# Optimization experiments

Hardware: AMD Instinct MI355X
Metric: run time of the kernel (lower is better)

## Reference

```python
import jax, jax.numpy as jnp
import numpy as np

D_MODEL = 1024
N_HEADS = 16
D_K = D_MODEL // N_HEADS
MAX_SEQ = 2048
THETA = 10000.0


def _make_cos_sin():
    # cos_sin[i, k, 0] = cos(i / theta**(2k/d_k)), [.., 1] = sin(...)
    pos = np.arange(MAX_SEQ, dtype=np.float32)[:, None]
    k = np.arange(D_K // 2, dtype=np.float32)[None, :]
    ang = pos / (THETA ** (2.0 * k / D_K))
    return jnp.asarray(np.stack([np.cos(ang), np.sin(ang)], axis=-1), dtype=jnp.float32)


def setup_inputs() -> dict:
    key = jax.random.key(0)
    ks = jax.random.split(key, 5)
    std = 2.0 / (D_MODEL + D_MODEL)
    def w(k):
        return std * jax.random.truncated_normal(k, -3.0, 3.0, (D_MODEL, D_MODEL), dtype=jnp.float32)
    return {
        "x": jax.random.normal(ks[0], (4, 2048, D_MODEL), dtype=jnp.float32),
        "Wq": w(ks[1]),
        "Wk": w(ks[2]),
        "Wv": w(ks[3]),
        "Wo": w(ks[4]),
        "cos_sin": _make_cos_sin(),
        "token_positions": jnp.arange(2048, dtype=jnp.int32),
    }


def _rope(x, cos_sin, pos):
    # x: [B, H, S, d_k]; rotate consecutive pairs
    B, H, S, d = x.shape
    xt = x.reshape(B, H, S, d // 2, 2)
    cos = cos_sin[pos, :, 0]  # [S, d/2]
    sin = cos_sin[pos, :, 1]
    x0, x1 = xt[..., 0], xt[..., 1]
    r0 = cos * x0 - sin * x1
    r1 = sin * x0 + cos * x1
    return jnp.stack([r0, r1], axis=-1).reshape(B, H, S, d)


def reference(x, Wq, Wk, Wv, Wo, cos_sin, token_positions):
    B, S, D = x.shape
    H, d = N_HEADS, D_K
    def proj(W):
        y = jnp.einsum('bsi,oi->bso', x, W)
        return y.reshape(B, S, H, d).transpose(0, 2, 1, 3)  # [B,H,S,d]
    q = _rope(proj(Wq), cos_sin, token_positions)
    k = _rope(proj(Wk), cos_sin, token_positions)
    v = proj(Wv)
    scores = jnp.einsum('bhqd,bhkd->bhqk', q, k) / jnp.sqrt(jnp.float32(d))
    causal = jnp.tril(jnp.ones((S, S), dtype=bool))
    scores = jnp.where(causal, scores, -jnp.inf)
    attn = jax.nn.softmax(scores, axis=-1)
    out = jnp.einsum('bhqk,bhkd->bhqd', attn, v)
    out = out.transpose(0, 2, 1, 3).reshape(B, S, D)
    return jnp.einsum('bsi,oi->bso', out, Wo)
```

## Files before the change

### kernel.cpp

```cpp
#include <hip/hip_runtime.h>

constexpr int B_  = 4;
constexpr int S_  = 2048;
constexpr int D_  = 1024;
constexpr int H_  = 16;
constexpr int DK_ = 64;
constexpr int M_  = B_ * S_;

typedef __attribute__((ext_vector_type(8))) short short8;
typedef __attribute__((ext_vector_type(4))) float f32x4;
typedef __attribute__((ext_vector_type(4))) unsigned short us4;

__device__ __forceinline__ unsigned short f2b(float f) {
  unsigned int u = __float_as_uint(f);
  u += 0x7FFFu + ((u >> 16) & 1u);
  return (unsigned short)(u >> 16);
}
__device__ __forceinline__ float b2f(unsigned short h) {
  return __uint_as_float(((unsigned int)h) << 16);
}
__device__ __forceinline__ unsigned int cvtpk(float lo, float hi) {
  unsigned int w;
  asm("v_cvt_pk_bf16_f32 %0, %1, %2" : "=v"(w) : "v"(lo), "v"(hi));
  return w;
}
__device__ __forceinline__ float exp2v(float x) {
  float r;
  asm("v_exp_f32 %0, %1" : "=v"(r) : "v"(x));
  return r;
}

#define GLOAD16(g, l) __builtin_amdgcn_global_load_lds( \
    (const __attribute__((address_space(1))) unsigned int*)(g), \
    (__attribute__((address_space(3))) unsigned int*)(l), 16, 0, 0)

__global__ __launch_bounds__(256) void conv_kernel(
    const float* __restrict__ x,
    const float* __restrict__ wq, const float* __restrict__ wk, const float* __restrict__ wv,
    unsigned short* __restrict__ xb, unsigned short* __restrict__ wb)
{
  const int NX4 = (M_ * D_) / 4;
  const int NW4 = (3 * D_ * D_) / 4;
  int stride = gridDim.x * blockDim.x;
  for (int i = blockIdx.x * blockDim.x + threadIdx.x; i < NX4 + NW4; i += stride) {
    const float4* src; unsigned short* dst; int o;
    if (i < NX4) { src = (const float4*)x; dst = xb; o = i; }
    else {
      int wi = i - NX4;
      int mat = wi >> 18;
      o = wi & 262143;
      src = (const float4*)(mat == 0 ? wq : (mat == 1 ? wk : wv));
      dst = wb + mat * (D_ * D_);
    }
    float4 v = src[o];
    us4 r; r.x = f2b(v.x); r.y = f2b(v.y); r.z = f2b(v.z); r.w = f2b(v.w);
    *(us4*)(dst + o * 4) = r;
  }
}

__global__ __launch_bounds__(256) void conv_wo_kernel(
    const float* __restrict__ wo, unsigned short* __restrict__ wob)
{
  int i = blockIdx.x * 256 + threadIdx.x;
  float4 v = ((const float4*)wo)[i];
  us4 r; r.x = f2b(v.x); r.y = f2b(v.y); r.z = f2b(v.z); r.w = f2b(v.w);
  *(us4*)(wob + i * 4) = r;
}

__global__ __launch_bounds__(256) void gemm_qkv_kernel(
    const unsigned short* __restrict__ xb,
    const unsigned short* __restrict__ wb,
    const float* __restrict__ cs,
    const int* __restrict__ pos,
    unsigned short* __restrict__ qb,
    unsigned short* __restrict__ kb,
    unsigned short* __restrict__ vtb)
{
  __shared__ unsigned short As[128 * 32];
  __shared__ unsigned short Bs[128 * 32];
  const int tid  = threadIdx.x;
  const int lane = tid & 63;
  const int wid  = tid >> 6;
  const int wm = wid >> 1, wn = wid & 1;
  const int m0 = blockIdx.x * 128;
  const int n0 = blockIdx.y * 128;
  const int l15 = lane & 15, l4 = lane >> 4;

  const int c0 = tid;
  const int rA0 = c0 >> 2, cA0 = (c0 & 3) * 8;
  const int c1 = tid + 256;
  const int rA1 = c1 >> 2, cA1 = (c1 & 3) * 8;
  const int lb0 = (wid * 64) * 8;
  const int lb1 = (256 + wid * 64) * 8;

  f32x4 acc[4][4] = {};

  for (int t = 0; t < 32; ++t) {
    __syncthreads();
    GLOAD16(xb + (m0 + rA0) * D_ + t * 32 + cA0, &As[lb0]);
    GLOAD16(xb + (m0 + rA1) * D_ + t * 32 + cA1, &As[lb1]);
    GLOAD16(wb + (n0 + rA0) * D_ + t * 32 + cA0, &Bs[lb0]);
    GLOAD16(wb + (n0 + rA1) * D_ + t * 32 + cA1, &Bs[lb1]);
    __syncthreads();

    short8 af[4], bfr[4];
    #pragma unroll
    for (int mi = 0; mi < 4; ++mi) af[mi]  = *(const short8*)&As[(wm*64 + mi*16 + l15)*32 + l4*8];
    #pragma unroll
    for (int ni = 0; ni < 4; ++ni) bfr[ni] = *(const short8*)&Bs[(wn*64 + ni*16 + l15)*32 + l4*8];
    __builtin_amdgcn_s_setprio(1);
    #pragma unroll
    for (int mi = 0; mi < 4; ++mi)
      #pragma unroll
      for (int ni = 0; ni < 4; ++ni)
        acc[mi][ni] = __builtin_amdgcn_mfma_f32_16x16x32_bf16(af[mi], bfr[ni], acc[mi][ni], 0, 0, 0);
    __builtin_amdgcn_s_setprio(0);
  }

  const int bidx = m0 >> 11;
  const int sbase = (m0 & 2047) + wm * 64;

  if (n0 < 2048) {
    unsigned short* dst = (n0 < 1024) ? qb : kb;
    const int nn0 = n0 & 1023;
    const float2* cs2 = (const float2*)cs;
    const float sg = (l15 & 1) ? 1.0f : -1.0f;
    #pragma unroll
    for (int mi = 0; mi < 4; ++mi)
      #pragma unroll
      for (int j = 0; j < 4; ++j) {
        int s = sbase + mi*16 + l4*4 + j;
        int p = pos[s];
        #pragma unroll
        for (int ni = 0; ni < 4; ++ni) {
          int col = nn0 + wn*64 + ni*16 + l15;
          int h = col >> 6, dd = col & 63;
          float val = acc[mi][ni][j];
          float par = __shfl_xor(val, 1);
          float2 cv = cs2[p*32 + (dd >> 1)];
          float r = fmaf(cv.x, val, sg * cv.y * par);
          dst[((bidx*H_ + h)*S_ + s)*DK_ + dd] = f2b(r);
        }
      }
  } else {
    const int nn0 = n0 & 1023;
    const int hB = (nn0 + wn*64) >> 6;
    #pragma unroll
    for (int mi = 0; mi < 4; ++mi) {
      int s4 = sbase + mi*16 + l4*4;
      #pragma unroll
      for (int ni = 0; ni < 4; ++ni) {
        int dd = ni*16 + l15;
        uint2 w;
        w.x = cvtpk(acc[mi][ni][0], acc[mi][ni][1]);
        w.y = cvtpk(acc[mi][ni][2], acc[mi][ni][3]);
        *(uint2*)(vtb + ((bidx*H_ + hB)*DK_ + dd)*S_ + s4) = w;
      }
    }
  }
}

__global__ __launch_bounds__(256, 4) void attn_kernel(
    const unsigned short* __restrict__ qb,
    const unsigned short* __restrict__ kb,
    const unsigned short* __restrict__ vtb,
    unsigned short* __restrict__ ao)
{
  __shared__ unsigned short Ks[64][72];
  __shared__ unsigned short Vs[64][72];
  __shared__ unsigned short Ps[4][16][72];
  const int tid = threadIdx.x, lane = tid & 63, wid = tid >> 6;
  const int l15 = lane & 15, l4 = lane >> 4;

  const int id  = blockIdx.x;
  const int xcd = id & 7, jj2 = id >> 3;
  const int bh  = xcd * 8 + (jj2 & 7);
  const int qt  = 15 - (jj2 >> 3);
  const int q0  = qt * 128;
  const int nkt = 2 * qt + 2;

  const unsigned short* qp = qb  + bh * S_ * DK_;
  const unsigned short* kp = kb  + bh * S_ * DK_;
  const unsigned short* vp = vtb + bh * DK_ * S_;
  const int bidx = bh >> 4, h = bh & 15;

  const float QSC = 0.18033688f;
  short8 qf[2][2];
  #pragma unroll
  for (int y = 0; y < 2; ++y)
    #pragma unroll
    for (int kbk = 0; kbk < 2; ++kbk) {
      short8 raw = *(const short8*)(qp + (q0 + y*64 + wid*16 + l15)*DK_ + kbk*32 + l4*8);
      #pragma unroll
      for (int i = 0; i < 8; ++i) {
        float f = b2f((unsigned short)raw[i]) * QSC;
        raw[i] = (short)f2b(f);
      }
      qf[y][kbk] = raw;
    }

  f32x4 oacc[2][4] = {};
  float mrun[2] = {-1e30f, -1e30f}, lrun[2] = {0.0f, 0.0f};

  short8 kv[2], vv[2];
  #pragma unroll
  for (int jj = 0; jj < 2; ++jj) {
    int c = tid + jj * 256;
    int r = c >> 3, col = (c & 7) * 8;
    kv[jj] = *(const short8*)(kp + r*DK_ + col);
    vv[jj] = *(const short8*)(vp + r*S_ + col);
  }

  for (int kt = 0; kt < nkt; ++kt) {
    __syncthreads();
    #pragma unroll
    for (int jj = 0; jj < 2; ++jj) {
      int c = tid + jj * 256;
      int r = c >> 3, col = (c & 7) * 8;
      *(short8*)&Ks[r][col] = kv[jj];
      *(short8*)&Vs[r][col] = vv[jj];
    }
    __syncthreads();

    if (kt + 1 < nkt) {
      #pragma unroll
      for (int jj = 0; jj < 2; ++jj) {
        int c = tid + jj * 256;
        int r = c >> 3, col = (c & 7) * 8;
        kv[jj] = *(const short8*)(kp + ((kt+1)*64 + r)*DK_ + col);
        vv[jj] = *(const short8*)(vp + r*S_ + (kt+1)*64 + col);
      }
    }

    #pragma unroll
    for (int y = 0; y < 2; ++y) {
      if (kt > 2*qt + y) continue;

      f32x4 sc[4];
      __builtin_amdgcn_s_setprio(1);
      #pragma unroll
      for (int nb = 0; nb < 4; ++nb) {
        short8 k0 = *(const short8*)&Ks[nb*16 + l15][l4*8];
        short8 k1 = *(const short8*)&Ks[nb*16 + l15][32 + l4*8];
        f32x4 z = {};
        z = __builtin_amdgcn_mfma_f32_16x16x32_bf16(k0, qf[y][0], z, 0, 0, 0);
        z = __builtin_amdgcn_mfma_f32_16x16x32_bf16(k1, qf[y][1], z, 0, 0, 0);
        sc[nb] = z;
      }
      __builtin_amdgcn_s_setprio(0);

      if (kt == 2*qt + y) {
        const int qg = q0 + y*64 + wid*16 + l15;
        #pragma unroll
        for (int nb = 0; nb < 4; ++nb)
          #pragma unroll
          for (int j = 0; j < 4; ++j) {
            int kg = kt*64 + nb*16 + l4*4 + j;
            if (kg > qg) sc[nb][j] = -1e30f;
          }
      }

      float tm = sc[0][0];
      #pragma unroll
      for (int nb = 0; nb < 4; ++nb)
        #pragma unroll
        for (int j = 0; j < 4; ++j) tm = fmaxf(tm, sc[nb][j]);
      tm = fmaxf(tm, __shfl_xor(tm, 16));
      tm = fmaxf(tm, __shfl_xor(tm, 32));
      if (!__all(tm - mrun[y] <= 8.0f)) {
        float mnew = fmaxf(mrun[y], tm);
        float corr = exp2v(mrun[y] - mnew);
        mrun[y] = mnew;
        lrun[y] *= corr;
        #pragma unroll
        for (int j = 0; j < 4; ++j) {
          float cj = __shfl(corr, l4*4 + j);
          #pragma unroll
          for (int nb = 0; nb < 4; ++nb) oacc[y][nb][j] *= cj;
        }
      }
      float rs = 0.0f;
      #pragma unroll
      for (int nb = 0; nb < 4; ++nb)
        #pragma unroll
        for (int j = 0; j < 4; ++j) {
          float p = exp2v(sc[nb][j] - mrun[y]);
          sc[nb][j] = p;
          rs += p;
        }
      rs += __shfl_xor(rs, 16);
      rs += __shfl_xor(rs, 32);
      lrun[y] += rs;

      #pragma unroll
      for (int nb = 0; nb < 4; ++nb) {
        uint2 w;
        w.x = cvtpk(sc[nb][0], sc[nb][1]);
        w.y = cvtpk(sc[nb][2], sc[nb][3]);
        *(uint2*)&Ps[wid][l15][nb*16 + l4*4] = w;
      }
      asm volatile("s_waitcnt lgkmcnt(0)" ::: "memory");
      short8 pa0 = *(const short8*)&Ps[wid][l15][l4*8];
      short8 pa1 = *(const short8*)&Ps[wid][l15][32 + l4*8];

      __builtin_amdgcn_s_setprio(1);
      #pragma unroll
      for (int nb = 0; nb < 4; ++nb) {
        short8 v0 = *(const short8*)&Vs[nb*16 + l15][l4*8];
        short8 v1 = *(const short8*)&Vs[nb*16 + l15][32 + l4*8];
        oacc[y][nb] = __builtin_amdgcn_mfma_f32_16x16x32_bf16(pa0, v0, oacc[y][nb], 0, 0, 0);
        oacc[y][nb] = __builtin_amdgcn_mfma_f32_16x16x32_bf16(pa1, v1, oacc[y][nb], 0, 0, 0);
      }
      __builtin_amdgcn_s_setprio(0);
    }
  }

  #pragma unroll
  for (int y = 0; y < 2; ++y)
    #pragma unroll
    for (int j = 0; j < 4; ++j) {
      float lj = __shfl(lrun[y], l4*4 + j);
      float inv = 1.0f / lj;
      int row = q0 + y*64 + wid*16 + l4*4 + j;
      #pragma unroll
      for (int nb = 0; nb < 4; ++nb) {
        int dim = nb*16 + l15;
        ao[((bidx*S_ + row)*H_ + h)*DK_ + dim] = f2b(oacc[y][nb][j] * inv);
      }
    }
}

__global__ __launch_bounds__(256) void gemm_out_kernel(
    const unsigned short* __restrict__ ao,
    const unsigned short* __restrict__ wob,
    float* __restrict__ out)
{
  __shared__ unsigned short As[128 * 32];
  __shared__ unsigned short Bs[128 * 32];
  const int tid = threadIdx.x, lane = tid & 63, wid = tid >> 6;
  const int wm = wid >> 1, wn = wid & 1;
  const int m0 = blockIdx.x * 128, n0 = blockIdx.y * 128;
  const int l15 = lane & 15, l4 = lane >> 4;

  const int c0 = tid;
  const int rA0 = c0 >> 2, cA0 = (c0 & 3) * 8;
  const int c1 = tid + 256;
  const int rA1 = c1 >> 2, cA1 = (c1 & 3) * 8;
  const int lb0 = (wid * 64) * 8;
  const int lb1 = (256 + wid * 64) * 8;

  f32x4 acc[4][4] = {};

  for (int t = 0; t < 32; ++t) {
    __syncthreads();
    GLOAD16(ao  + (m0 + rA0) * D_ + t * 32 + cA0, &As[lb0]);
    GLOAD16(ao  + (m0 + rA1) * D_ + t * 32 + cA1, &As[lb1]);
    GLOAD16(wob + (n0 + rA0) * D_ + t * 32 + cA0, &Bs[lb0]);
    GLOAD16(wob + (n0 + rA1) * D_ + t * 32 + cA1, &Bs[lb1]);
    __syncthreads();

    short8 af[4], bfr[4];
    #pragma unroll
    for (int mi = 0; mi < 4; ++mi) af[mi]  = *(const short8*)&As[(wm*64 + mi*16 + l15)*32 + l4*8];
    #pragma unroll
    for (int ni = 0; ni < 4; ++ni) bfr[ni] = *(const short8*)&Bs[(wn*64 + ni*16 + l15)*32 + l4*8];
    __builtin_amdgcn_s_setprio(1);
    #pragma unroll
    for (int mi = 0; mi < 4; ++mi)
      #pragma unroll
      for (int ni = 0; ni < 4; ++ni)
        acc[mi][ni] = __builtin_amdgcn_mfma_f32_16x16x32_bf16(af[mi], bfr[ni], acc[mi][ni], 0, 0, 0);
    __builtin_amdgcn_s_setprio(0);
  }

  #pragma unroll
  for (int mi = 0; mi < 4; ++mi)
    #pragma unroll
    for (int ni = 0; ni < 4; ++ni)
      #pragma unroll
      for (int j = 0; j < 4; ++j) {
        int row = m0 + wm*64 + mi*16 + l4*4 + j;
        int col = n0 + wn*64 + ni*16 + l15;
        out[row * D_ + col] = acc[mi][ni][j];
      }
}

extern "C" void kernel_launch(void* const* d_in, const int* in_sizes, int n_in,
                              void* d_out, int out_size, void* d_ws, size_t ws_size,
                              hipStream_t stream)
{
  const float* x  = (const float*)d_in[0];
  const float* wq = (const float*)d_in[1];
  const float* wk = (const float*)d_in[2];
  const float* wv = (const float*)d_in[3];
  const float* wo = (const float*)d_in[4];
  const float* cs = (const float*)d_in[5];
  const int*  pos = (const int*)d_in[6];
  float* out = (float*)d_out;

  unsigned short* xb = (unsigned short*)d_out;
  unsigned short* wb = xb + M_ * D_;

  unsigned short* qb  = (unsigned short*)d_ws;
  unsigned short* kbf = qb  + M_ * D_;
  unsigned short* vtb = kbf + M_ * D_;
  unsigned short* aob = vtb + M_ * D_;
  unsigned short* wob = qb;

  conv_kernel<<<dim3(2048), dim3(256), 0, stream>>>(x, wq, wk, wv, xb, wb);
  gemm_qkv_kernel<<<dim3(64, 24), dim3(256), 0, stream>>>(xb, wb, cs, pos, qb, kbf, vtb);
  attn_kernel<<<dim3(1024), dim3(256), 0, stream>>>(qb, kbf, vtb, aob);
  conv_wo_kernel<<<dim3(1024), dim3(256), 0, stream>>>(wo, wob);
  gemm_out_kernel<<<dim3(64, 8), dim3(256), 0, stream>>>(aob, wob, out);

  (void)in_sizes; (void)n_in; (void)out_size; (void)ws_size;
}
```

Baseline: 201.9 us.

## Double-buffer GEMM LDS tiles with BK=64 and XOR swizzle

Both projection GEMMs (QKV and output) now stage 64-wide K tiles in double-buffered LDS. The next tile's global-to-LDS loads are issued before the current tile's MFMAs, so there is one barrier per iteration instead of two. Tile columns are XOR-swizzled by row to avoid LDS bank conflicts on the 128-byte row stride, and launch bounds request two blocks per CU. The cost is four times the LDS per block (64 KB), which may limit occupancy. It also relies on async loads not landing early in the buffer still being read.

```diff
diff --git a/kernel.cpp b/kernel.cpp
--- a/kernel.cpp
+++ b/kernel.cpp
@@ -67,7 +67,7 @@
   *(us4*)(wob + i * 4) = r;
 }
 
-__global__ __launch_bounds__(256) void gemm_qkv_kernel(
+__global__ __launch_bounds__(256, 2) void gemm_qkv_kernel(
     const unsigned short* __restrict__ xb,
     const unsigned short* __restrict__ wb,
     const float* __restrict__ cs,
@@ -76,8 +76,8 @@
     unsigned short* __restrict__ kb,
     unsigned short* __restrict__ vtb)
 {
-  __shared__ unsigned short As[128 * 32];
-  __shared__ unsigned short Bs[128 * 32];
+  __shared__ unsigned short As[2][128 * 64];
+  __shared__ unsigned short Bs[2][128 * 64];
   const int tid  = threadIdx.x;
   const int lane = tid & 63;
   const int wid  = tid >> 6;
@@ -85,36 +85,56 @@
   const int m0 = blockIdx.x * 128;
   const int n0 = blockIdx.y * 128;
   const int l15 = lane & 15, l4 = lane >> 4;
-
-  const int c0 = tid;
-  const int rA0 = c0 >> 2, cA0 = (c0 & 3) * 8;
-  const int c1 = tid + 256;
-  const int rA1 = c1 >> 2, cA1 = (c1 & 3) * 8;
-  const int lb0 = (wid * 64) * 8;
-  const int lb1 = (256 + wid * 64) * 8;
+  const int swz7 = l15 & 7;
+
+  int srow[4], sgcc[4], slds[4];
+  #pragma unroll
+  for (int j = 0; j < 4; ++j) {
+    int c = tid + j * 256;
+    srow[j] = c >> 3;
+    int cc  = c & 7;
+    sgcc[j] = cc ^ (srow[j] & 7);
+    slds[j] = (wid * 64 + j * 256) * 8;
+  }
 
   f32x4 acc[4][4] = {};
 
-  for (int t = 0; t < 32; ++t) {
+  #pragma unroll
+  for (int j = 0; j < 4; ++j) {
+    GLOAD16(xb + (m0 + srow[j]) * D_ + sgcc[j] * 8, &As[0][slds[j]]);
+    GLOAD16(wb + (n0 + srow[j]) * D_ + sgcc[j] * 8, &Bs[0][slds[j]]);
+  }
+  __syncthreads();
+
+  for (int t = 0; t < 16; ++t) {
+    const int cur = t & 1, nxt = cur ^ 1;
+    if (t < 15) {
+      const int kcol = (t + 1) * 64;
+      #pragma unroll
+      for (int j = 0; j < 4; ++j) {
+        GLOAD16(xb + (m0 + srow[j]) * D_ + kcol + sgcc[j] * 8, &As[nxt][slds[j]]);
+        GLOAD16(wb + (n0 + srow[j]) * D_ + kcol + sgcc[j] * 8, &Bs[nxt][slds[j]]);
+      }
+    }
+    const unsigned short* Ab = &As[cur][0];
+    const unsigned short* Bb = &Bs[cur][0];
+    #pragma unroll
+    for (int ks = 0; ks < 2; ++ks) {
+      const int cc = (ks * 4 + l4) ^ swz7;
+      short8 af[4], bfr[4];
+      #pragma unroll
+      for (int mi = 0; mi < 4; ++mi) af[mi]  = *(const short8*)&Ab[(wm*64 + mi*16 + l15)*64 + cc*8];
+      #pragma unroll
+      for (int ni = 0; ni < 4; ++ni) bfr[ni] = *(const short8*)&Bb[(wn*64 + ni*16 + l15)*64 + cc*8];
+      __builtin_amdgcn_s_setprio(1);
+      #pragma unroll
+      for (int mi = 0; mi < 4; ++mi)
+        #pragma unroll
+        for (int ni = 0; ni < 4; ++ni)
+          acc[mi][ni] = __builtin_amdgcn_mfma_f32_16x16x32_bf16(af[mi], bfr[ni], acc[mi][ni], 0, 0, 0);
+      __builtin_amdgcn_s_setprio(0);
+    }
     __syncthreads();
-    GLOAD16(xb + (m0 + rA0) * D_ + t * 32 + cA0, &As[lb0]);
-    GLOAD16(xb + (m0 + rA1) * D_ + t * 32 + cA1, &As[lb1]);
-    GLOAD16(wb + (n0 + rA0) * D_ + t * 32 + cA0, &Bs[lb0]);
-    GLOAD16(wb + (n0 + rA1) * D_ + t * 32 + cA1, &Bs[lb1]);
-    __syncthreads();
-
-    short8 af[4], bfr[4];
-    #pragma unroll
-    for (int mi = 0; mi < 4; ++mi) af[mi]  = *(const short8*)&As[(wm*64 + mi*16 + l15)*32 + l4*8];
-    #pragma unroll
-    for (int ni = 0; ni < 4; ++ni) bfr[ni] = *(const short8*)&Bs[(wn*64 + ni*16 + l15)*32 + l4*8];
-    __builtin_amdgcn_s_setprio(1);
-    #pragma unroll
-    for (int mi = 0; mi < 4; ++mi)
-      #pragma unroll
-      for (int ni = 0; ni < 4; ++ni)
-        acc[mi][ni] = __builtin_amdgcn_mfma_f32_16x16x32_bf16(af[mi], bfr[ni], acc[mi][ni], 0, 0, 0);
-    __builtin_amdgcn_s_setprio(0);
   }
 
   const int bidx = m0 >> 11;
@@ -330,47 +350,67 @@
     }
 }
 
-__global__ __launch_bounds__(256) void gemm_out_kernel(
+__global__ __launch_bounds__(256, 2) void gemm_out_kernel(
     const unsigned short* __restrict__ ao,
     const unsigned short* __restrict__ wob,
     float* __restrict__ out)
 {
-  __shared__ unsigned short As[128 * 32];
-  __shared__ unsigned short Bs[128 * 32];
+  __shared__ unsigned short As[2][128 * 64];
+  __shared__ unsigned short Bs[2][128 * 64];
   const int tid = threadIdx.x, lane = tid & 63, wid = tid >> 6;
   const int wm = wid >> 1, wn = wid & 1;
   const int m0 = blockIdx.x * 128, n0 = blockIdx.y * 128;
   const int l15 = lane & 15, l4 = lane >> 4;
-
-  const int c0 = tid;
-  const int rA0 = c0 >> 2, cA0 = (c0 & 3) * 8;
-  const int c1 = tid + 256;
-  const int rA1 = c1 >> 2, cA1 = (c1 & 3) * 8;
-  const int lb0 = (wid * 64) * 8;
-  const int lb1 = (256 + wid * 64) * 8;
+  const int swz7 = l15 & 7;
+
+  int srow[4], sgcc[4], slds[4];
+  #pragma unroll
+  for (int j = 0; j < 4; ++j) {
+    int c = tid + j * 256;
+    srow[j] = c >> 3;
+    int cc  = c & 7;
+    sgcc[j] = cc ^ (srow[j] & 7);
+    slds[j] = (wid * 64 + j * 256) * 8;
+  }
 
   f32x4 acc[4][4] = {};
 
-  for (int t = 0; t < 32; ++t) {
+  #pragma unroll
+  for (int j = 0; j < 4; ++j) {
+    GLOAD16(ao  + (m0 + srow[j]) * D_ + sgcc[j] * 8, &As[0][slds[j]]);
+    GLOAD16(wob + (n0 + srow[j]) * D_ + sgcc[j] * 8, &Bs[0][slds[j]]);
+  }
+  __syncthreads();
+
+  for (int t = 0; t < 16; ++t) {
+    const int cur = t & 1, nxt = cur ^ 1;
+    if (t < 15) {
+      const int kcol = (t + 1) * 64;
+      #pragma unroll
+      for (int j = 0; j < 4; ++j) {
+        GLOAD16(ao  + (m0 + srow[j]) * D_ + kcol + sgcc[j] * 8, &As[nxt][slds[j]]);
+        GLOAD16(wob + (n0 + srow[j]) * D_ + kcol + sgcc[j] * 8, &Bs[nxt][slds[j]]);
+      }
+    }
+    const unsigned short* Ab = &As[cur][0];
+    const unsigned short* Bb = &Bs[cur][0];
+    #pragma unroll
+    for (int ks = 0; ks < 2; ++ks) {
+      const int cc = (ks * 4 + l4) ^ swz7;
+      short8 af[4], bfr[4];
+      #pragma unroll
+      for (int mi = 0; mi < 4; ++mi) af[mi]  = *(const short8*)&Ab[(wm*64 + mi*16 + l15)*64 + cc*8];
+      #pragma unroll
+      for (int ni = 0; ni < 4; ++ni) bfr[ni] = *(const short8*)&Bb[(wn*64 + ni*16 + l15)*64 + cc*8];
+      __builtin_amdgcn_s_setprio(1);
+      #pragma unroll
+      for (int mi = 0; mi < 4; ++mi)
+        #pragma unroll
+        for (int ni = 0; ni < 4; ++ni)
+          acc[mi][ni] = __builtin_amdgcn_mfma_f32_16x16x32_bf16(af[mi], bfr[ni], acc[mi][ni], 0, 0, 0);
+      __builtin_amdgcn_s_setprio(0);
+    }
     __syncthreads();
-    GLOAD16(ao  + (m0 + rA0) * D_ + t * 32 + cA0, &As[lb0]);
-    GLOAD16(ao  + (m0 + rA1) * D_ + t * 32 + cA1, &As[lb1]);
-    GLOAD16(wob + (n0 + rA0) * D_ + t * 32 + cA0, &Bs[lb0]);
-    GLOAD16(wob + (n0 + rA1) * D_ + t * 32 + cA1, &Bs[lb1]);
-    __syncthreads();
-
-    short8 af[4], bfr[4];
-    #pragma unroll
-    for (int mi = 0; mi < 4; ++mi) af[mi]  = *(const short8*)&As[(wm*64 + mi*16 + l15)*32 + l4*8];
-    #pragma unroll
-    for (int ni = 0; ni < 4; ++ni) bfr[ni] = *(const short8*)&Bs[(wn*64 + ni*16 + l15)*32 + l4*8];
-    __builtin_amdgcn_s_setprio(1);
-    #pragma unroll
-    for (int mi = 0; mi < 4; ++mi)
-      #pragma unroll
-      for (int ni = 0; ni < 4; ++ni)
-        acc[mi][ni] = __builtin_amdgcn_mfma_f32_16x16x32_bf16(af[mi], bfr[ni], acc[mi][ni], 0, 0, 0);
-    __builtin_amdgcn_s_setprio(0);
   }
 
   #pragma unroll
```

Measured after the change: 184.9 us. 8.4% less time.
